# Kernel optimization log

Hardware: AMD Instinct MI355X
Metric: run time of the kernel (lower is better)

The kernel has to match this reference:

```python
import jax, jax.numpy as jnp
import numpy as np

EMBED_DIM = 1024
NUM_HEADS = 16
HEAD_DIM = EMBED_DIM // NUM_HEADS
B, S = 4, 1024
EPS = 1e-5
NEG = -1e9


def layer_norm(h, gamma, beta):
    mu = jnp.mean(h, axis=-1, keepdims=True)
    var = jnp.mean(jnp.square(h - mu), axis=-1, keepdims=True)
    return (h - mu) * jax.lax.rsqrt(var + EPS) * gamma + beta


def setup_inputs() -> dict:
    key = jax.random.key(0)
    ks = jax.random.split(key, 8)
    scale = 1.0 / np.sqrt(EMBED_DIM)
    x = jax.random.normal(ks[0], (B, S, EMBED_DIM), dtype=jnp.float32)
    mask = jax.random.randint(ks[1], (B, S, S), 0, 2).astype(jnp.bool_)
    Wq = jax.random.uniform(ks[2], (EMBED_DIM, EMBED_DIM), jnp.float32, -scale, scale)
    bq = jax.random.uniform(ks[3], (EMBED_DIM,), jnp.float32, -scale, scale)
    Wk = jax.random.uniform(ks[4], (EMBED_DIM, EMBED_DIM), jnp.float32, -scale, scale)
    bk = jax.random.uniform(ks[5], (EMBED_DIM,), jnp.float32, -scale, scale)
    gq = jnp.ones((EMBED_DIM,), jnp.float32)
    bq_n = jnp.zeros((EMBED_DIM,), jnp.float32)
    gk = jnp.ones((EMBED_DIM,), jnp.float32)
    bk_n = jnp.zeros((EMBED_DIM,), jnp.float32)
    return {"x": x, "mask": mask, "Wq": Wq, "bq": bq, "Wk": Wk, "bk": bk,
            "gq": gq, "bq_n": bq_n, "gk": gk, "bk_n": bk_n}


def reference(x, mask, Wq, bq, Wk, bk, gq, bq_n, gk, bk_n):
    b, s, _ = x.shape
    # proj -> LayerNorm -> ReLU, split heads: [B,S,H,D]
    Q = jax.nn.relu(layer_norm(x @ Wq + bq, gq, bq_n)).reshape(b, s, NUM_HEADS, HEAD_DIM)
    K = jax.nn.relu(layer_norm(x @ Wk + bk, gk, bk_n)).reshape(b, s, NUM_HEADS, HEAD_DIM)
    # scores [B,H,S,S]
    scores = jnp.einsum('bqhd,bkhd->bhqk', Q, K) / np.sqrt(HEAD_DIM).astype(np.float32)
    # symmetric masking: mask applied along keys, then (via transpose trick) along queries
    m = (mask | jnp.swapaxes(mask, -1, -2))[:, None, :, :]
    scores = jnp.where(m, NEG, scores)
    attn = jax.nn.softmax(scores, axis=-1)
    return attn.mean(axis=1)  # [B,S,S]
```

## Files before the change

kernel.cpp:

```cpp
#include <hip/hip_runtime.h>
#include <hip/hip_bf16.h>

#define B_ 4
#define S_ 1024
#define E_ 1024
#define H_ 16
#define D_ 64

typedef __attribute__((ext_vector_type(8))) short short8;
typedef __attribute__((ext_vector_type(4))) float f32x4;

static __device__ __forceinline__ unsigned short f2bf(float x) {
  unsigned int u = __float_as_uint(x);
  unsigned int r = u + 0x7fffu + ((u >> 16) & 1u);
  return (unsigned short)(r >> 16);
}
static __device__ __forceinline__ float bf2f(unsigned short b) {
  return __uint_as_float((unsigned int)b << 16);
}

#define GL2LDS16(g, l)                                                            \
  __builtin_amdgcn_global_load_lds(                                               \
      (const __attribute__((address_space(1))) unsigned int*)(g),                 \
      (__attribute__((address_space(3))) unsigned int*)(l), 16, 0, 0)

__global__ __launch_bounds__(256) void prep_kernel(const int* __restrict__ mask,
                                                   const float* __restrict__ x,
                                                   const float* __restrict__ Wq,
                                                   const float* __restrict__ Wk,
                                                   unsigned char* __restrict__ msym,
                                                   unsigned short* __restrict__ xbf,
                                                   unsigned short* __restrict__ Wt) {
  __shared__ __align__(16) char u_lds[32 * 33 * 4];
  const int blk = blockIdx.x;
  const int tid = threadIdx.x;
  if (blk < 4096) {
    int (*T)[33] = (int(*)[33])u_lds;
    const int b = blk >> 10;
    const int rest = blk & 1023;
    const int i0 = (rest >> 5) << 5;
    const int j0 = (rest & 31) << 5;
    const int ii = tid >> 3;
    const int jj4 = (tid & 7) << 2;
    const size_t bO = (size_t)b * S_ * S_;
    const int4 m2 = *(const int4*)&mask[bO + (size_t)(j0 + ii) * S_ + i0 + jj4];
    T[ii][jj4 + 0] = m2.x; T[ii][jj4 + 1] = m2.y; T[ii][jj4 + 2] = m2.z; T[ii][jj4 + 3] = m2.w;
    __syncthreads();
    const int4 m1 = *(const int4*)&mask[bO + (size_t)(i0 + ii) * S_ + j0 + jj4];
    uchar4 o;
    o.x = ((m1.x != 0) || (T[jj4 + 0][ii] != 0)) ? 1 : 0;
    o.y = ((m1.y != 0) || (T[jj4 + 1][ii] != 0)) ? 1 : 0;
    o.z = ((m1.z != 0) || (T[jj4 + 2][ii] != 0)) ? 1 : 0;
    o.w = ((m1.w != 0) || (T[jj4 + 3][ii] != 0)) ? 1 : 0;
    *(uchar4*)&msym[bO + (size_t)(i0 + ii) * S_ + j0 + jj4] = o;
  } else if (blk < 6144) {
    const size_t i = ((size_t)(blk - 4096) * 256 + tid) * 8;
    const float4 a = *(const float4*)(x + i);
    const float4 b = *(const float4*)(x + i + 4);
    const ushort4 p0 = {f2bf(a.x), f2bf(a.y), f2bf(a.z), f2bf(a.w)};
    const ushort4 p1 = {f2bf(b.x), f2bf(b.y), f2bf(b.z), f2bf(b.w)};
    *(ushort4*)(xbf + i) = p0;
    *(ushort4*)(xbf + i + 4) = p1;
  } else {
    unsigned short (*T2)[36] = (unsigned short(*)[36])u_lds;
    const int wblk = blk - 6144;
    const int mat = wblk >> 10;
    const int kt = (wblk >> 5) & 31, ntb = wblk & 31;
    const float* W = mat ? Wk : Wq;
    const int r = tid >> 3, c4 = (tid & 7) << 2;
    const float4 v = *(const float4*)&W[(size_t)(kt * 32 + r) * 1024 + ntb * 32 + c4];
    T2[r][c4 + 0] = f2bf(v.x); T2[r][c4 + 1] = f2bf(v.y);
    T2[r][c4 + 2] = f2bf(v.z); T2[r][c4 + 3] = f2bf(v.w);
    __syncthreads();
    const ushort4 o = {T2[c4 + 0][r], T2[c4 + 1][r], T2[c4 + 2][r], T2[c4 + 3][r]};
    *(ushort4*)&Wt[(size_t)(mat * 1024 + ntb * 32 + r) * 1024 + kt * 32 + c4] = o;
  }
}

__global__ __launch_bounds__(256) void gemm_mfma_kernel(const unsigned short* __restrict__ Abf,
                                                        const unsigned short* __restrict__ Wt,
                                                        unsigned short* __restrict__ P,
                                                        int nstride) {
  __shared__ __align__(16) unsigned short As[128 * 64];
  __shared__ __align__(16) unsigned short Bs[128 * 64];
  const int tid = threadIdx.x;
  const int m0 = (blockIdx.x & 31) << 7;
  const int n0 = (blockIdx.x >> 5) << 7;
  const int wave = tid >> 6, lane = tid & 63;
  const int ln15 = lane & 15, rg = lane >> 4;
  const int wm = (wave & 1) << 6;
  const int wn = (wave >> 1) << 6;
  const int sr = tid >> 3;
  const int sc = (tid & 7) << 3;
  const unsigned short* gA = Abf + (size_t)(m0 + sr) * 1024 + sc;
  const unsigned short* gB = Wt + (size_t)(n0 + sr) * 1024 + sc;
  unsigned short* lA = As + tid * 8;
  unsigned short* lB = Bs + tid * 8;
  f32x4 acc[4][4];
#pragma unroll
  for (int i = 0; i < 4; ++i)
#pragma unroll
    for (int j = 0; j < 4; ++j) acc[i][j] = (f32x4){0.0f, 0.0f, 0.0f, 0.0f};

  const unsigned short* pa = As + (wm + ln15) * 64 + rg * 8;
  const unsigned short* pb = Bs + (wn + ln15) * 64 + rg * 8;
  for (int k0 = 0; k0 < E_; k0 += 64) {
#pragma unroll
    for (int j = 0; j < 4; ++j) {
      GL2LDS16(gA + k0 + (size_t)(j * 32) * 1024, lA + j * 2048);
      GL2LDS16(gB + k0 + (size_t)(j * 32) * 1024, lB + j * 2048);
    }
    __syncthreads();
#pragma unroll
    for (int kk = 0; kk < 2; ++kk) {
      short8 af[4], bfr[4];
#pragma unroll
      for (int i = 0; i < 4; ++i) af[i] = *(const short8*)(pa + i * 16 * 64 + kk * 32);
#pragma unroll
      for (int j = 0; j < 4; ++j) bfr[j] = *(const short8*)(pb + j * 16 * 64 + kk * 32);
#pragma unroll
      for (int i = 0; i < 4; ++i)
#pragma unroll
        for (int j = 0; j < 4; ++j)
          acc[i][j] = __builtin_amdgcn_mfma_f32_16x16x32_bf16(af[i], bfr[j], acc[i][j], 0, 0, 0);
    }
    __syncthreads();
  }
#pragma unroll
  for (int i = 0; i < 4; ++i)
#pragma unroll
    for (int j = 0; j < 4; ++j)
#pragma unroll
      for (int r = 0; r < 4; ++r) {
        const int row = m0 + wm + i * 16 + rg * 4 + r;
        const int col = n0 + wn + j * 16 + ln15;
        P[(size_t)row * nstride + col] = f2bf(acc[i][j][r]);
      }
}

__device__ __forceinline__ void ln_body(const unsigned short* p, const float* bias,
                                        const float* gamma, const float* beta,
                                        unsigned short* obf, int b, int s, int tid) {
  const ushort4 pv = *(const ushort4*)(p + tid * 4);
  float4 v = {bf2f(pv.x), bf2f(pv.y), bf2f(pv.z), bf2f(pv.w)};
  const float4 bb = ((const float4*)bias)[tid];
  v.x += bb.x; v.y += bb.y; v.z += bb.z; v.w += bb.w;
  float sum = v.x + v.y + v.z + v.w;
  float s2 = v.x * v.x + v.y * v.y + v.z * v.z + v.w * v.w;
#pragma unroll
  for (int off = 32; off >= 1; off >>= 1) {
    sum += __shfl_xor(sum, off);
    s2 += __shfl_xor(s2, off);
  }
  __shared__ float red[2][4];
  const int wave = tid >> 6, lane = tid & 63;
  if (lane == 0) { red[0][wave] = sum; red[1][wave] = s2; }
  __syncthreads();
  sum = red[0][0] + red[0][1] + red[0][2] + red[0][3];
  s2 = red[1][0] + red[1][1] + red[1][2] + red[1][3];
  const float mu = sum * (1.0f / E_);
  const float var = s2 * (1.0f / E_) - mu * mu;
  const float r = rsqrtf(var + 1e-5f);
  const float4 g = ((const float4*)gamma)[tid];
  const float4 bt = ((const float4*)beta)[tid];
  const float o0 = fmaxf((v.x - mu) * r * g.x + bt.x, 0.0f);
  const float o1 = fmaxf((v.y - mu) * r * g.y + bt.y, 0.0f);
  const float o2 = fmaxf((v.z - mu) * r * g.z + bt.z, 0.0f);
  const float o3 = fmaxf((v.w - mu) * r * g.w + bt.w, 0.0f);
  const int h = tid >> 4;
  const int d = (tid & 15) << 2;
  const ushort4 ob = {f2bf(o0), f2bf(o1), f2bf(o2), f2bf(o3)};
  *(ushort4*)&obf[((size_t)(b * H_ + h) * S_ + s) * D_ + d] = ob;
}

__global__ __launch_bounds__(256) void ln_relu_bf_kernel(const unsigned short* __restrict__ P,
                                                         int rowstride, int coloff,
                                                         const float* __restrict__ bias,
                                                         const float* __restrict__ gamma,
                                                         const float* __restrict__ beta,
                                                         unsigned short* __restrict__ obf) {
  const int row = blockIdx.x;
  ln_body(P + (size_t)row * rowstride + coloff, bias, gamma, beta, obf,
          row >> 10, row & 1023, threadIdx.x);
}

__global__ __launch_bounds__(256) void ln2_kernel(const unsigned short* __restrict__ P2,
                                                  const float* __restrict__ bq,
                                                  const float* __restrict__ gq,
                                                  const float* __restrict__ bqn,
                                                  const float* __restrict__ bk,
                                                  const float* __restrict__ gk,
                                                  const float* __restrict__ bkn,
                                                  unsigned short* __restrict__ Qbf,
                                                  unsigned short* __restrict__ Kbf) {
  const int blk = blockIdx.x;
  const int sel = blk >> 12;
  const int row = blk & 4095;
  ln_body(P2 + (size_t)row * 2048 + sel * 1024,
          sel ? bk : bq, sel ? gk : gq, sel ? bkn : bqn,
          sel ? Kbf : Qbf, row >> 10, row & 1023, threadIdx.x);
}

__global__ __launch_bounds__(1024, 4) void attn8_kernel(const unsigned short* __restrict__ Qbf,
                                                        const unsigned short* __restrict__ Kbf,
                                                        const unsigned char* __restrict__ msym,
                                                        float* __restrict__ out) {
  __shared__ __align__(16) unsigned short Ks[2][512 * 64];
  __shared__ __align__(16) float l_lds[16][16];
  __shared__ __align__(16) float linv[16];
  const int tid = threadIdx.x;
  const int wave = tid >> 6, lane = tid & 63;
  const int ln15 = lane & 15, rg = lane >> 4;
  const int b = blockIdx.x & 3;
  const int q0 = (blockIdx.x >> 2) << 4;
  const unsigned short* Kb = Kbf + (size_t)b * H_ * S_ * D_;
  const unsigned short* Qb = Qbf + (size_t)b * H_ * S_ * D_;

  unsigned int mbits = 0;
#pragma unroll
  for (int half = 0; half < 2; ++half)
#pragma unroll
    for (int jt = 0; jt < 2; ++jt)
#pragma unroll
      for (int r = 0; r < 4; ++r)
        mbits |= (msym[((size_t)b * S_ + q0 + rg * 4 + r) * S_ + half * 512 + wave * 32 + jt * 16 + ln15]
                      ? 1u : 0u) << (half * 8 + jt * 4 + r);

  const int skey = tid >> 3;
  const int sgc = ((tid & 7) ^ (skey & 7)) << 3;
#pragma unroll
  for (int c = 0; c < 4; ++c)
    GL2LDS16(Kb + (size_t)(c * 128 + skey) * D_ + sgc, Ks[0] + c * 8192 + tid * 8);
  __syncthreads();

  const int pfrag = (rg ^ (ln15 & 7)) * 8;
  float o[2][2][4] = {};
  float ef[2][2][4];
  float la[4];

#pragma unroll 1
  for (int h = 0; h < 16; ++h) {
    const unsigned short* qrow = Qb + ((size_t)h * S_ + q0 + ln15) * D_ + rg * 8;
    const short8 a0 = *(const short8*)qrow;
    const short8 a1 = *(const short8*)(qrow + 32);
    la[0] = la[1] = la[2] = la[3] = 0.0f;
#pragma unroll
    for (int half = 0; half < 2; ++half) {
      const int s = h * 2 + half;
      if (s < 31) {
        const int h1 = (s + 1) >> 1, hf1 = (s + 1) & 1;
        const unsigned short* g = Kb + (size_t)h1 * (S_ * D_) + (size_t)(hf1 * 512 + skey) * D_ + sgc;
        unsigned short* lp = Ks[(s + 1) & 1] + tid * 8;
#pragma unroll
        for (int c = 0; c < 4; ++c)
          GL2LDS16(g + (size_t)(c * 128) * D_, lp + c * 8192);
      }
      const unsigned short* kw = Ks[s & 1] + (wave * 32 + ln15) * 64;
#pragma unroll
      for (int jt = 0; jt < 2; ++jt) {
        const unsigned short* kp = kw + jt * 16 * 64;
        const short8 b0 = *(const short8*)(kp + pfrag);
        const short8 b1 = *(const short8*)(kp + (pfrag ^ 32));
        f32x4 cc = {0.0f, 0.0f, 0.0f, 0.0f};
        cc = __builtin_amdgcn_mfma_f32_16x16x32_bf16(a0, b0, cc, 0, 0, 0);
        cc = __builtin_amdgcn_mfma_f32_16x16x32_bf16(a1, b1, cc, 0, 0, 0);
#pragma unroll
        for (int r = 0; r < 4; ++r) {
          const float sv = fminf(cc[r] * 0.125f, 80.0f);
          const float ev = ((mbits >> (half * 8 + jt * 4 + r)) & 1u) ? 0.0f : __expf(sv);
          ef[half][jt][r] = ev;
          la[r] += ev;
        }
      }
      if (half == 0) {
        __syncthreads();
      } else {
#pragma unroll
        for (int r = 0; r < 4; ++r) {
          float lv = la[r];
          lv += __shfl_xor(lv, 1);
          lv += __shfl_xor(lv, 2);
          lv += __shfl_xor(lv, 4);
          lv += __shfl_xor(lv, 8);
          la[r] = lv;
        }
        if (ln15 == 0) *(float4*)&l_lds[wave][rg * 4] = (float4){la[0], la[1], la[2], la[3]};
        __syncthreads();
        if (tid < 16) {
          float ssum = 0.0f;
#pragma unroll
          for (int w = 0; w < 16; ++w) ssum += l_lds[w][tid];
          linv[tid] = 0.0625f / ssum;
        }
        __syncthreads();
        const float4 li4 = *(const float4*)&linv[rg * 4];
#pragma unroll
        for (int hf = 0; hf < 2; ++hf)
#pragma unroll
          for (int jt = 0; jt < 2; ++jt) {
            o[hf][jt][0] += ef[hf][jt][0] * li4.x;
            o[hf][jt][1] += ef[hf][jt][1] * li4.y;
            o[hf][jt][2] += ef[hf][jt][2] * li4.z;
            o[hf][jt][3] += ef[hf][jt][3] * li4.w;
          }
      }
    }
  }
#pragma unroll
  for (int half = 0; half < 2; ++half)
#pragma unroll
    for (int jt = 0; jt < 2; ++jt)
#pragma unroll
      for (int r = 0; r < 4; ++r)
        out[((size_t)b * S_ + q0 + rg * 4 + r) * S_ + half * 512 + wave * 32 + jt * 16 + ln15] =
            o[half][jt][r];
}

extern "C" void kernel_launch(void* const* d_in, const int* in_sizes, int n_in,
                              void* d_out, int out_size, void* d_ws, size_t ws_size,
                              hipStream_t stream) {
  const float* x = (const float*)d_in[0];
  const int* mask = (const int*)d_in[1];
  const float* Wq = (const float*)d_in[2];
  const float* bq = (const float*)d_in[3];
  const float* Wk = (const float*)d_in[4];
  const float* bk = (const float*)d_in[5];
  const float* gq = (const float*)d_in[6];
  const float* bq_n = (const float*)d_in[7];
  const float* gk = (const float*)d_in[8];
  const float* bk_n = (const float*)d_in[9];
  float* out = (float*)d_out;

  char* ws = (char*)d_ws;
  const size_t MB = 1024 * 1024;

  if (ws_size >= 40 * MB) {
    unsigned short* P2 = (unsigned short*)ws;
    unsigned short* xbf = (unsigned short*)(ws + 16 * MB);
    unsigned short* Kbf = (unsigned short*)(ws + 16 * MB);
    unsigned short* Wt = (unsigned short*)(ws + 24 * MB);
    unsigned short* Qbf = (unsigned short*)(ws + 28 * MB);
    unsigned char* msym = (unsigned char*)(ws + 36 * MB);

    prep_kernel<<<8192, 256, 0, stream>>>(mask, x, Wq, Wk, msym, xbf, Wt);
    gemm_mfma_kernel<<<512, 256, 0, stream>>>(xbf, Wt, P2, 2048);
    ln2_kernel<<<8192, 256, 0, stream>>>(P2, bq, gq, bq_n, bk, gk, bk_n, Qbf, Kbf);
    attn8_kernel<<<256, 1024, 0, stream>>>(Qbf, Kbf, msym, out);
  } else {
    unsigned short* P = (unsigned short*)ws;
    unsigned short* xbf = (unsigned short*)(ws + 8 * MB);
    unsigned short* Kbf = (unsigned short*)(ws + 8 * MB);
    unsigned short* Wt = (unsigned short*)(ws + 16 * MB);
    unsigned short* Qbf = (unsigned short*)(ws + 20 * MB);
    unsigned char* msym = (unsigned char*)(ws + 28 * MB);

    prep_kernel<<<8192, 256, 0, stream>>>(mask, x, Wq, Wk, msym, xbf, Wt);
    gemm_mfma_kernel<<<256, 256, 0, stream>>>(xbf, Wt, P, 1024);
    ln_relu_bf_kernel<<<4096, 256, 0, stream>>>(P, 1024, 0, bq, gq, bq_n, Qbf);
    gemm_mfma_kernel<<<256, 256, 0, stream>>>(xbf, Wt + (size_t)1024 * 1024, P, 1024);
    ln_relu_bf_kernel<<<4096, 256, 0, stream>>>(P, 1024, 0, bk, gk, bk_n, Kbf);
    attn8_kernel<<<256, 1024, 0, stream>>>(Qbf, Kbf, msym, out);
  }
}
```

Measured before the change: 197.2 us.

## Make K staging per-wave private and cut attention barriers to one per head

Each wave now loads its own 32-key slice of K into a private LDS region and waits with vmcnt instead of a block-wide barrier. Only the cross-wave softmax denominator exchange stays synchronized, through a double-buffered l_lds and a shuffle reduction, with an rcp in place of a division. This removes two or three __syncthreads per head to reduce barrier stalls in the attention kernel. The hand-coded waitcnt encoding has to match the number of outstanding loads, or LDS reads may race.

```diff
diff --git a/kernel.cpp b/kernel.cpp
--- a/kernel.cpp
+++ b/kernel.cpp
@@ -23,6 +23,8 @@
   __builtin_amdgcn_global_load_lds(                                               \
       (const __attribute__((address_space(1))) unsigned int*)(g),                 \
       (__attribute__((address_space(3))) unsigned int*)(l), 16, 0, 0)
+
+#define WAIT_VMCNT4() __builtin_amdgcn_s_waitcnt(0x0F74)
 
 __global__ __launch_bounds__(256) void prep_kernel(const int* __restrict__ mask,
                                                    const float* __restrict__ x,
@@ -201,13 +203,12 @@
           sel ? Kbf : Qbf, row >> 10, row & 1023, threadIdx.x);
 }
 
-__global__ __launch_bounds__(1024, 4) void attn8_kernel(const unsigned short* __restrict__ Qbf,
+__global__ __launch_bounds__(1024, 4) void attn9_kernel(const unsigned short* __restrict__ Qbf,
                                                         const unsigned short* __restrict__ Kbf,
                                                         const unsigned char* __restrict__ msym,
                                                         float* __restrict__ out) {
-  __shared__ __align__(16) unsigned short Ks[2][512 * 64];
-  __shared__ __align__(16) float l_lds[16][16];
-  __shared__ __align__(16) float linv[16];
+  __shared__ __align__(16) unsigned short Ks[2][16][2048];
+  __shared__ __align__(16) float l_lds[2][16][16];
   const int tid = threadIdx.x;
   const int wave = tid >> 6, lane = tid & 63;
   const int ln15 = lane & 15, rg = lane >> 4;
@@ -218,20 +219,20 @@
 
   unsigned int mbits = 0;
 #pragma unroll
-  for (int half = 0; half < 2; ++half)
+  for (int hf = 0; hf < 2; ++hf)
 #pragma unroll
     for (int jt = 0; jt < 2; ++jt)
 #pragma unroll
       for (int r = 0; r < 4; ++r)
-        mbits |= (msym[((size_t)b * S_ + q0 + rg * 4 + r) * S_ + half * 512 + wave * 32 + jt * 16 + ln15]
-                      ? 1u : 0u) << (half * 8 + jt * 4 + r);
-
-  const int skey = tid >> 3;
-  const int sgc = ((tid & 7) ^ (skey & 7)) << 3;
-#pragma unroll
-  for (int c = 0; c < 4; ++c)
-    GL2LDS16(Kb + (size_t)(c * 128 + skey) * D_ + sgc, Ks[0] + c * 8192 + tid * 8);
-  __syncthreads();
+        mbits |= (msym[((size_t)b * S_ + q0 + rg * 4 + r) * S_ + hf * 512 + wave * 32 + jt * 16 + ln15]
+                      ? 1u : 0u) << (hf * 8 + jt * 4 + r);
+
+  const int gl = ((lane >> 3) << 6) + (((lane & 7) ^ (lane >> 3)) << 3);
+  const unsigned short* gwave = Kb + wave * 2048 + gl;
+#pragma unroll
+  for (int c = 0; c < 4; ++c) GL2LDS16(gwave + c * 512, &Ks[0][wave][c * 512]);
+#pragma unroll
+  for (int c = 0; c < 4; ++c) GL2LDS16(gwave + 32768 + c * 512, &Ks[1][wave][c * 512]);
 
   const int pfrag = (rg ^ (ln15 & 7)) * 8;
   float o[2][2][4] = {};
@@ -245,20 +246,20 @@
     const short8 a1 = *(const short8*)(qrow + 32);
     la[0] = la[1] = la[2] = la[3] = 0.0f;
 #pragma unroll
-    for (int half = 0; half < 2; ++half) {
-      const int s = h * 2 + half;
+    for (int hf = 0; hf < 2; ++hf) {
+      const int s = h * 2 + hf;
       if (s < 31) {
-        const int h1 = (s + 1) >> 1, hf1 = (s + 1) & 1;
-        const unsigned short* g = Kb + (size_t)h1 * (S_ * D_) + (size_t)(hf1 * 512 + skey) * D_ + sgc;
-        unsigned short* lp = Ks[(s + 1) & 1] + tid * 8;
-#pragma unroll
-        for (int c = 0; c < 4; ++c)
-          GL2LDS16(g + (size_t)(c * 128) * D_, lp + c * 8192);
+        const int s1 = s + 1;
+        const unsigned short* g = gwave + (size_t)(s1 >> 1) * 65536 + (s1 & 1) * 32768;
+        unsigned short* lp = &Ks[s1 & 1][wave][0];
+#pragma unroll
+        for (int c = 0; c < 4; ++c) GL2LDS16(g + c * 512, lp + c * 512);
       }
-      const unsigned short* kw = Ks[s & 1] + (wave * 32 + ln15) * 64;
+      if (s == 0 || (s & 1)) WAIT_VMCNT4();
+      const unsigned short* kw = &Ks[s & 1][wave][ln15 * 64];
 #pragma unroll
       for (int jt = 0; jt < 2; ++jt) {
-        const unsigned short* kp = kw + jt * 16 * 64;
+        const unsigned short* kp = kw + jt * 1024;
         const short8 b0 = *(const short8*)(kp + pfrag);
         const short8 b1 = *(const short8*)(kp + (pfrag ^ 32));
         f32x4 cc = {0.0f, 0.0f, 0.0f, 0.0f};
@@ -267,53 +268,51 @@
 #pragma unroll
         for (int r = 0; r < 4; ++r) {
           const float sv = fminf(cc[r] * 0.125f, 80.0f);
-          const float ev = ((mbits >> (half * 8 + jt * 4 + r)) & 1u) ? 0.0f : __expf(sv);
-          ef[half][jt][r] = ev;
+          const float ev = ((mbits >> (hf * 8 + jt * 4 + r)) & 1u) ? 0.0f : __expf(sv);
+          ef[hf][jt][r] = ev;
           la[r] += ev;
         }
       }
-      if (half == 0) {
-        __syncthreads();
-      } else {
-#pragma unroll
-        for (int r = 0; r < 4; ++r) {
-          float lv = la[r];
-          lv += __shfl_xor(lv, 1);
-          lv += __shfl_xor(lv, 2);
-          lv += __shfl_xor(lv, 4);
-          lv += __shfl_xor(lv, 8);
-          la[r] = lv;
-        }
-        if (ln15 == 0) *(float4*)&l_lds[wave][rg * 4] = (float4){la[0], la[1], la[2], la[3]};
-        __syncthreads();
-        if (tid < 16) {
-          float ssum = 0.0f;
-#pragma unroll
-          for (int w = 0; w < 16; ++w) ssum += l_lds[w][tid];
-          linv[tid] = 0.0625f / ssum;
-        }
-        __syncthreads();
-        const float4 li4 = *(const float4*)&linv[rg * 4];
-#pragma unroll
-        for (int hf = 0; hf < 2; ++hf)
-#pragma unroll
-          for (int jt = 0; jt < 2; ++jt) {
-            o[hf][jt][0] += ef[hf][jt][0] * li4.x;
-            o[hf][jt][1] += ef[hf][jt][1] * li4.y;
-            o[hf][jt][2] += ef[hf][jt][2] * li4.z;
-            o[hf][jt][3] += ef[hf][jt][3] * li4.w;
-          }
-      }
-    }
-  }
-#pragma unroll
-  for (int half = 0; half < 2; ++half)
+    }
+#pragma unroll
+    for (int r = 0; r < 4; ++r) {
+      float lv = la[r];
+      lv += __shfl_xor(lv, 1);
+      lv += __shfl_xor(lv, 2);
+      lv += __shfl_xor(lv, 4);
+      lv += __shfl_xor(lv, 8);
+      la[r] = lv;
+    }
+    if (ln15 == 0) *(float4*)&l_lds[h & 1][wave][rg * 4] = (float4){la[0], la[1], la[2], la[3]};
+    __syncthreads();
+    const float4 pw = *(const float4*)&l_lds[h & 1][ln15][rg * 4];
+    float p[4] = {pw.x, pw.y, pw.z, pw.w};
+#pragma unroll
+    for (int r = 0; r < 4; ++r) {
+      float lv = p[r];
+      lv += __shfl_xor(lv, 1);
+      lv += __shfl_xor(lv, 2);
+      lv += __shfl_xor(lv, 4);
+      lv += __shfl_xor(lv, 8);
+      p[r] = lv;
+    }
+#pragma unroll
+    for (int r = 0; r < 4; ++r) {
+      const float li = 0.0625f * __builtin_amdgcn_rcpf(p[r]);
+#pragma unroll
+      for (int hf = 0; hf < 2; ++hf)
+#pragma unroll
+        for (int jt = 0; jt < 2; ++jt) o[hf][jt][r] += ef[hf][jt][r] * li;
+    }
+  }
+#pragma unroll
+  for (int hf = 0; hf < 2; ++hf)
 #pragma unroll
     for (int jt = 0; jt < 2; ++jt)
 #pragma unroll
       for (int r = 0; r < 4; ++r)
-        out[((size_t)b * S_ + q0 + rg * 4 + r) * S_ + half * 512 + wave * 32 + jt * 16 + ln15] =
-            o[half][jt][r];
+        out[((size_t)b * S_ + q0 + rg * 4 + r) * S_ + hf * 512 + wave * 32 + jt * 16 + ln15] =
+            o[hf][jt][r];
 }
 
 extern "C" void kernel_launch(void* const* d_in, const int* in_sizes, int n_in,
@@ -345,7 +344,7 @@
     prep_kernel<<<8192, 256, 0, stream>>>(mask, x, Wq, Wk, msym, xbf, Wt);
     gemm_mfma_kernel<<<512, 256, 0, stream>>>(xbf, Wt, P2, 2048);
     ln2_kernel<<<8192, 256, 0, stream>>>(P2, bq, gq, bq_n, bk, gk, bk_n, Qbf, Kbf);
-    attn8_kernel<<<256, 1024, 0, stream>>>(Qbf, Kbf, msym, out);
+    attn9_kernel<<<256, 1024, 0, stream>>>(Qbf, Kbf, msym, out);
   } else {
     unsigned short* P = (unsigned short*)ws;
     unsigned short* xbf = (unsigned short*)(ws + 8 * MB);
@@ -359,6 +358,6 @@
     ln_relu_bf_kernel<<<4096, 256, 0, stream>>>(P, 1024, 0, bq, gq, bq_n, Qbf);
     gemm_mfma_kernel<<<256, 256, 0, stream>>>(xbf, Wt + (size_t)1024 * 1024, P, 1024);
     ln_relu_bf_kernel<<<4096, 256, 0, stream>>>(P, 1024, 0, bk, gk, bk_n, Kbf);
-    attn8_kernel<<<256, 1024, 0, stream>>>(Qbf, Kbf, msym, out);
-  }
-}
+    attn9_kernel<<<256, 1024, 0, stream>>>(Qbf, Kbf, msym, out);
+  }
+}
```

New measurement: 194.2 us. Within noise of the previous version (-1.5%).
